# Optimization experiments

Measured on AMD Instinct MI355X. Metric: run time of the kernel, lower is better.

## Reference

```python
import jax, jax.numpy as jnp
import numpy as np

HIDDEN = 1024
B, S = 4, 2048

def setup_inputs() -> dict:
    key = jax.random.key(0)
    ks = jax.random.split(key, 8)
    scale = 1.0 / np.sqrt(HIDDEN)
    return {
        "x": jax.random.normal(ks[0], (B, S, HIDDEN), dtype=jnp.float32),
        "mask": jax.random.randint(ks[1], (B, S, S), 0, 2, dtype=jnp.int32),
        "Wq": jax.random.normal(ks[2], (HIDDEN, HIDDEN), dtype=jnp.float32) * scale,
        "bq": jax.random.normal(ks[3], (HIDDEN,), dtype=jnp.float32) * 0.01,
        "Wk": jax.random.normal(ks[4], (HIDDEN, HIDDEN), dtype=jnp.float32) * scale,
        "bk": jax.random.normal(ks[5], (HIDDEN,), dtype=jnp.float32) * 0.01,
        "Wv": jax.random.normal(ks[6], (HIDDEN, HIDDEN), dtype=jnp.float32) * scale,
        "bv": jax.random.normal(ks[7], (HIDDEN,), dtype=jnp.float32) * 0.01,
    }

def reference(x, mask, Wq, bq, Wk, bk, Wv, bv):
    # torch Linear: y = x @ W.T + b
    Q = jnp.einsum("bsh,oh->bso", x, Wq) + bq
    K = jnp.einsum("bsh,oh->bso", x, Wk) + bk
    V = jnp.einsum("bsh,oh->bso", x, Wv) + bv
    inv_sqrt_h = 1.0 / jnp.sqrt(jnp.asarray(Q.shape[-1], Q.dtype))
    score = jnp.einsum("bqh,bkh->bqk", Q, K) * inv_sqrt_h  # [B, S, S]
    score = jnp.where(mask == 0, jnp.asarray(-jnp.inf, score.dtype), score)
    attn = jax.nn.softmax(score, axis=-1)
    return jnp.einsum("bqk,bkh->bqh", attn, V)
```

## Files before the change

kernel.cpp:

```cpp
#include <hip/hip_runtime.h>

using u16 = unsigned short;
using u32 = unsigned int;

typedef __attribute__((ext_vector_type(4))) float f32x4;
typedef __attribute__((ext_vector_type(8))) short s16x8;

__device__ __forceinline__ u16 f2b(float f) {
  u32 u = __builtin_bit_cast(u32, f);
  u += 0x7FFFu + ((u >> 16) & 1u);
  return (u16)(u >> 16);
}
__device__ __forceinline__ float b2f(u16 h) {
  return __builtin_bit_cast(float, (u32)h << 16);
}
__device__ __forceinline__ void gl_lds16(const void* g, void* l) {
  __builtin_amdgcn_global_load_lds(
      (const __attribute__((address_space(1))) void*)g,
      (__attribute__((address_space(3))) void*)l, 16, 0, 0);
}
template<int N> __device__ __forceinline__ void waitvm() {
  static_assert(N == 8 || N == 6 || N == 4 || N == 3 || N == 0, "literal");
  if constexpr (N == 8)      asm volatile("s_waitcnt vmcnt(8)" ::: "memory");
  else if constexpr (N == 6) asm volatile("s_waitcnt vmcnt(6)" ::: "memory");
  else if constexpr (N == 4) asm volatile("s_waitcnt vmcnt(4)" ::: "memory");
  else if constexpr (N == 3) asm volatile("s_waitcnt vmcnt(3)" ::: "memory");
  else                       asm volatile("s_waitcnt vmcnt(0)" ::: "memory");
}
__device__ __forceinline__ void barrier_np() {
  __builtin_amdgcn_s_barrier();
  asm volatile("" ::: "memory");
}

__global__ __launch_bounds__(256) void convert4_k(
    const float* __restrict__ x, const float* __restrict__ Wq,
    const float* __restrict__ Wk, const float* __restrict__ Wv,
    u16* __restrict__ dst) {
  long g = (long)(blockIdx.x * 256 + threadIdx.x) * 8;
  const float* s;
  if (g < 8388608L)       s = x  + g;
  else if (g < 9437184L)  s = Wq + (g - 8388608L);
  else if (g < 10485760L) s = Wk + (g - 9437184L);
  else                    s = Wv + (g - 10485760L);
  f32x4 lo = *(const f32x4*)s;
  f32x4 hi = *(const f32x4*)(s + 4);
  s16x8 o;
  #pragma unroll
  for (int e = 0; e < 4; ++e) { o[e] = (short)f2b(lo[e]); o[4 + e] = (short)f2b(hi[e]); }
  *(s16x8*)(dst + g) = o;
}

template<int EPI, int MREP>
__global__ __launch_bounds__(512, 2) void gemm_nt(
    const u16* __restrict__ A, const u16* __restrict__ B0,
    const u16* __restrict__ W2, const u16* __restrict__ W3,
    int lda, int ldb, int K, long za, long zb, long ze,
    const float* __restrict__ bq, const float* __restrict__ bk, const float* __restrict__ bv,
    u16* __restrict__ qw, u16* __restrict__ kw, u16* __restrict__ vt,
    const int* __restrict__ mask, u16* __restrict__ sc, float* __restrict__ outO)
{
  constexpr int BM    = 32 * MREP;
  constexpr int ACH   = BM * 4;
  constexpr int CH    = ACH + 1024;
  constexpr int CALLS = CH / 512;
  constexpr int BUF   = CH * 8;
  __shared__ __align__(16) u16 lds[4 * BUF];

  const int tid  = threadIdx.x;
  const int wave = tid >> 6, lane = tid & 63;
  const int wr = wave >> 2, wc = wave & 3;
  const int m0 = blockIdx.y * BM, n0 = blockIdx.x * 256;
  const long z = blockIdx.z;
  A += z * za;

  const u16* Bsrc = B0;
  int nbase = n0;
  if constexpr (EPI == 0) {
    Bsrc = (n0 < 1024) ? B0 : (n0 < 2048) ? W2 : W3;
    nbase = n0 & 1023;
  }
  Bsrc += z * zb;

  const u16* gsrc[CALLS];
  u32 loff[CALLS];
  #pragma unroll
  for (int call = 0; call < CALLS; ++call) {
    int qq  = call * 512 + tid;
    int isB = qq >= ACH;
    int r   = (isB ? qq - ACH : qq) >> 2;
    int kc  = (qq & 3) ^ (r & 3);
    gsrc[call] = isB ? (Bsrc + (size_t)(nbase + r) * ldb + kc * 8)
                     : (A    + (size_t)(m0    + r) * lda + kc * 8);
    loff[call] = (u32)qq * 8;
  }

  const int frow = lane & 15;
  const int q    = lane >> 4;
  u32 aoff[MREP], boff[4];
  #pragma unroll
  for (int i = 0; i < MREP; ++i) {
    int lr = wr * (16 * MREP) + i * 16 + frow;
    aoff[i] = (u32)lr * 32 + (u32)((q ^ (lr & 3)) << 3);
  }
  #pragma unroll
  for (int j = 0; j < 4; ++j) {
    int lc = wc * 64 + j * 16 + frow;
    boff[j] = (u32)ACH * 8 + (u32)lc * 32 + (u32)((q ^ (lc & 3)) << 3);
  }

  f32x4 acc[MREP][4];
  const f32x4 fz = {0.f, 0.f, 0.f, 0.f};
  #pragma unroll
  for (int i = 0; i < MREP; ++i)
    #pragma unroll
    for (int j = 0; j < 4; ++j) acc[i][j] = fz;

  const int NT = K >> 5;

  auto stage = [&](int t) {
    u16* buf = lds + (size_t)(t & 3) * BUF;
    #pragma unroll
    for (int call = 0; call < CALLS; ++call)
      gl_lds16(gsrc[call] + (size_t)t * 32, buf + loff[call]);
  };
  auto comp = [&](int t) {
    const u16* buf = lds + (size_t)(t & 3) * BUF;
    s16x8 bf[4];
    #pragma unroll
    for (int j = 0; j < 4; ++j) bf[j] = *(const s16x8*)(buf + boff[j]);
    __builtin_amdgcn_s_setprio(1);
    #pragma unroll
    for (int i = 0; i < MREP; ++i) {
      s16x8 af = *(const s16x8*)(buf + aoff[i]);
      #pragma unroll
      for (int j = 0; j < 4; ++j)
        acc[i][j] = __builtin_amdgcn_mfma_f32_16x16x32_bf16(af, bf[j], acc[i][j], 0, 0, 0);
    }
    __builtin_amdgcn_s_setprio(0);
  };

  stage(0); stage(1); stage(2);
  for (int T = 0; T < NT - 3; ++T) {
    waitvm<2 * CALLS>();
    barrier_np();
    stage(T + 3);
    comp(T);
  }
  waitvm<2 * CALLS>(); barrier_np(); comp(NT - 3);
  waitvm<CALLS>();     barrier_np(); comp(NT - 2);
  waitvm<0>();         barrier_np(); comp(NT - 1);

  const int r0 = (lane >> 4) * 4;
  const int ccol = lane & 15;
  #pragma unroll
  for (int i = 0; i < MREP; ++i) {
    #pragma unroll
    for (int j = 0; j < 4; ++j) {
      #pragma unroll
      for (int r = 0; r < 4; ++r) {
        int R = m0 + wr * (16 * MREP) + i * 16 + r0 + r;
        int C = n0 + wc * 64 + j * 16 + ccol;
        float v = acc[i][j][r];
        if constexpr (EPI == 0) {
          int sec = C >> 10, nl = C & 1023;
          v += (sec == 0) ? bq[nl] : (sec == 1) ? bk[nl] : bv[nl];
          u16 o = f2b(v);
          int b = R >> 11, s = R & 2047;
          if (sec == 0)      qw[(size_t)R * 1024 + nl] = o;
          else if (sec == 1) kw[(size_t)R * 1024 + nl] = o;
          else               vt[(size_t)b * 2097152u + (size_t)nl * 2048 + s] = o;
        } else if constexpr (EPI == 1) {
          v *= 0.03125f;
          size_t idx = (size_t)(z * ze) + (size_t)R * 2048 + C;
          if (mask[idx] == 0) v = -__builtin_inff();
          sc[idx] = f2b(v);
        } else {
          outO[(size_t)(z * ze) + (size_t)R * 1024 + C] = v;
        }
      }
    }
  }
}

__global__ __launch_bounds__(256) void softmax_k(u16* __restrict__ Sc) {
  __shared__ float red[8];
  u16* p = Sc + (size_t)blockIdx.x * 2048;
  const int tid = threadIdx.x;
  const int lane = tid & 63, wv = tid >> 6;
  s16x8 u = *(const s16x8*)(p + tid * 8);
  float v[8];
  #pragma unroll
  for (int e = 0; e < 8; ++e) v[e] = b2f((u16)u[e]);
  float mx = v[0];
  #pragma unroll
  for (int e = 1; e < 8; ++e) mx = fmaxf(mx, v[e]);
  #pragma unroll
  for (int off = 32; off > 0; off >>= 1) mx = fmaxf(mx, __shfl_xor(mx, off));
  if (lane == 0) red[wv] = mx;
  __syncthreads();
  mx = fmaxf(fmaxf(red[0], red[1]), fmaxf(red[2], red[3]));
  float s = 0.f;
  #pragma unroll
  for (int e = 0; e < 8; ++e) { v[e] = __expf(v[e] - mx); s += v[e]; }
  #pragma unroll
  for (int off = 32; off > 0; off >>= 1) s += __shfl_xor(s, off);
  if (lane == 0) red[4 + wv] = s;
  __syncthreads();
  s = (red[4] + red[5]) + (red[6] + red[7]);
  float inv = 1.f / s;
  s16x8 o;
  #pragma unroll
  for (int e = 0; e < 8; ++e) o[e] = (short)f2b(v[e] * inv);
  *(s16x8*)(p + tid * 8) = o;
}

extern "C" void kernel_launch(void* const* d_in, const int* in_sizes, int n_in,
                              void* d_out, int out_size, void* d_ws, size_t ws_size,
                              hipStream_t stream) {
  const float* x  = (const float*)d_in[0];
  const int* mask = (const int*)d_in[1];
  const float* Wq = (const float*)d_in[2];
  const float* bq = (const float*)d_in[3];
  const float* Wk = (const float*)d_in[4];
  const float* bk = (const float*)d_in[5];
  const float* Wv = (const float*)d_in[6];
  const float* bv = (const float*)d_in[7];
  float* out = (float*)d_out;
  char* ws = (char*)d_ws;

  u16* xc  = (u16*)ws;
  u16* Wqc = (u16*)(ws + (16u << 20));
  u16* Wkc = (u16*)(ws + (18u << 20));
  u16* Wvc = (u16*)(ws + (20u << 20));
  u16* Qw  = (u16*)(ws + (22u << 20));
  u16* Kw  = (u16*)(ws + (38u << 20));
  u16* Vt  = (u16*)(ws + (54u << 20));
  u16* Sc  = (u16*)(ws + (70u << 20));

  convert4_k<<<5632, 256, 0, stream>>>(x, Wq, Wk, Wv, xc);

  gemm_nt<0, 4><<<dim3(12, 64, 1), 512, 0, stream>>>(
      xc, Wqc, Wkc, Wvc, 1024, 1024, 1024, 0, 0, 0,
      bq, bk, bv, Qw, Kw, Vt, nullptr, nullptr, nullptr);
  gemm_nt<1, 8><<<dim3(8, 8, 4), 512, 0, stream>>>(
      Qw, Kw, nullptr, nullptr, 1024, 1024, 1024, 2097152, 2097152, 4194304,
      nullptr, nullptr, nullptr, nullptr, nullptr, nullptr, mask, Sc, nullptr);
  softmax_k<<<8192, 256, 0, stream>>>(Sc);
  gemm_nt<2, 4><<<dim3(4, 16, 4), 512, 0, stream>>>(
      Sc, Vt, nullptr, nullptr, 2048, 2048, 2048, 4194304, 2097152, 2097152,
      nullptr, nullptr, nullptr, nullptr, nullptr, nullptr, nullptr, nullptr, out);
}
```

Before: 338.6 us.

## Split GEMM tile compute into two halves interleaved with staged loads and barriers

Restructures the GEMM main loop so each k-tile is processed in two halves. The global-to-LDS prefetch is split between them and issued after the LDS fragment reads, with an extra barrier per half, to spread memory issue across the MFMA work. It also changes the LDS swizzle to XOR on (row>>1)&3 to cut bank conflicts, and switches the QKV projection to MREP=8 (256-row tiles, half the blocks). The added barriers and larger tiles trade extra synchronisation and fewer blocks for better overlap and more reuse.

```diff
diff --git a/kernel.cpp b/kernel.cpp
--- a/kernel.cpp
+++ b/kernel.cpp
@@ -63,8 +63,10 @@
   constexpr int ACH   = BM * 4;
   constexpr int CH    = ACH + 1024;
   constexpr int CALLS = CH / 512;
-  constexpr int BUF   = CH * 8;
-  __shared__ __align__(16) u16 lds[4 * BUF];
+  constexpr int SA    = 2;
+  constexpr int SLOT  = CH * 8;
+  constexpr int HM    = MREP / 2;
+  __shared__ __align__(16) u16 lds[4 * SLOT];
 
   const int tid  = threadIdx.x;
   const int wave = tid >> 6, lane = tid & 63;
@@ -84,14 +86,14 @@
   const u16* gsrc[CALLS];
   u32 loff[CALLS];
   #pragma unroll
-  for (int call = 0; call < CALLS; ++call) {
-    int qq  = call * 512 + tid;
+  for (int c = 0; c < CALLS; ++c) {
+    int qq  = c * 512 + tid;
     int isB = qq >= ACH;
     int r   = (isB ? qq - ACH : qq) >> 2;
-    int kc  = (qq & 3) ^ (r & 3);
-    gsrc[call] = isB ? (Bsrc + (size_t)(nbase + r) * ldb + kc * 8)
-                     : (A    + (size_t)(m0    + r) * lda + kc * 8);
-    loff[call] = (u32)qq * 8;
+    int kc  = (qq & 3) ^ ((r >> 1) & 3);
+    gsrc[c] = (isB ? (Bsrc + (size_t)(nbase + r) * ldb)
+                   : (A    + (size_t)(m0    + r) * lda)) + kc * 8;
+    loff[c] = (u32)qq * 8;
   }
 
   const int frow = lane & 15;
@@ -100,12 +102,12 @@
   #pragma unroll
   for (int i = 0; i < MREP; ++i) {
     int lr = wr * (16 * MREP) + i * 16 + frow;
-    aoff[i] = (u32)lr * 32 + (u32)((q ^ (lr & 3)) << 3);
+    aoff[i] = (u32)lr * 32 + (u32)((q ^ ((lr >> 1) & 3)) << 3);
   }
   #pragma unroll
   for (int j = 0; j < 4; ++j) {
     int lc = wc * 64 + j * 16 + frow;
-    boff[j] = (u32)ACH * 8 + (u32)lc * 32 + (u32)((q ^ (lc & 3)) << 3);
+    boff[j] = (u32)ACH * 8 + (u32)lc * 32 + (u32)((q ^ ((lc >> 1) & 3)) << 3);
   }
 
   f32x4 acc[MREP][4];
@@ -117,38 +119,61 @@
 
   const int NT = K >> 5;
 
-  auto stage = [&](int t) {
-    u16* buf = lds + (size_t)(t & 3) * BUF;
-    #pragma unroll
-    for (int call = 0; call < CALLS; ++call)
-      gl_lds16(gsrc[call] + (size_t)t * 32, buf + loff[call]);
+  auto stage_full = [&](int t) {
+    u16* b = lds + (size_t)(t & 3) * SLOT;
+    #pragma unroll
+    for (int c = 0; c < CALLS; ++c)
+      gl_lds16(gsrc[c] + (size_t)t * 32, b + loff[c]);
   };
-  auto comp = [&](int t) {
-    const u16* buf = lds + (size_t)(t & 3) * BUF;
-    s16x8 bf[4];
+
+  s16x8 bf[4];
+  auto tile_body = [&](int T, bool do_stage) {
+    const u16* buf = lds + (size_t)(T & 3) * SLOT;
+    u16* sb = lds + (size_t)((T + 3) & 3) * SLOT;
+    const size_t koff = (size_t)(T + 3) * 32;
+    s16x8 af[HM];
     #pragma unroll
     for (int j = 0; j < 4; ++j) bf[j] = *(const s16x8*)(buf + boff[j]);
+    #pragma unroll
+    for (int i = 0; i < HM; ++i) af[i] = *(const s16x8*)(buf + aoff[i]);
+    if (do_stage) {
+      #pragma unroll
+      for (int c = 0; c < SA; ++c) gl_lds16(gsrc[c] + koff, sb + loff[c]);
+    }
+    barrier_np();
     __builtin_amdgcn_s_setprio(1);
     #pragma unroll
-    for (int i = 0; i < MREP; ++i) {
-      s16x8 af = *(const s16x8*)(buf + aoff[i]);
+    for (int i = 0; i < HM; ++i)
       #pragma unroll
       for (int j = 0; j < 4; ++j)
-        acc[i][j] = __builtin_amdgcn_mfma_f32_16x16x32_bf16(af, bf[j], acc[i][j], 0, 0, 0);
+        acc[i][j] = __builtin_amdgcn_mfma_f32_16x16x32_bf16(af[i], bf[j], acc[i][j], 0, 0, 0);
+    __builtin_amdgcn_s_setprio(0);
+    s16x8 ag[HM];
+    #pragma unroll
+    for (int i = 0; i < HM; ++i) ag[i] = *(const s16x8*)(buf + aoff[HM + i]);
+    if (do_stage) {
+      #pragma unroll
+      for (int c = SA; c < CALLS; ++c) gl_lds16(gsrc[c] + koff, sb + loff[c]);
     }
+    barrier_np();
+    __builtin_amdgcn_s_setprio(1);
+    #pragma unroll
+    for (int i = 0; i < HM; ++i)
+      #pragma unroll
+      for (int j = 0; j < 4; ++j)
+        acc[HM + i][j] = __builtin_amdgcn_mfma_f32_16x16x32_bf16(ag[i], bf[j], acc[HM + i][j], 0, 0, 0);
     __builtin_amdgcn_s_setprio(0);
   };
 
-  stage(0); stage(1); stage(2);
+  stage_full(0); stage_full(1); stage_full(2);
   for (int T = 0; T < NT - 3; ++T) {
     waitvm<2 * CALLS>();
     barrier_np();
-    stage(T + 3);
-    comp(T);
-  }
-  waitvm<2 * CALLS>(); barrier_np(); comp(NT - 3);
-  waitvm<CALLS>();     barrier_np(); comp(NT - 2);
-  waitvm<0>();         barrier_np(); comp(NT - 1);
+    tile_body(T, true);
+  }
+  waitvm<2 * CALLS>(); barrier_np(); tile_body(NT - 3, false);
+  waitvm<CALLS>();     barrier_np(); tile_body(NT - 2, false);
+  waitvm<0>();         barrier_np(); tile_body(NT - 1, false);
 
   const int r0 = (lane >> 4) * 4;
   const int ccol = lane & 15;
@@ -239,7 +264,7 @@
 
   convert4_k<<<5632, 256, 0, stream>>>(x, Wq, Wk, Wv, xc);
 
-  gemm_nt<0, 4><<<dim3(12, 64, 1), 512, 0, stream>>>(
+  gemm_nt<0, 8><<<dim3(12, 32, 1), 512, 0, stream>>>(
       xc, Wqc, Wkc, Wvc, 1024, 1024, 1024, 0, 0, 0,
       bq, bk, bv, Qw, Kw, Vt, nullptr, nullptr, nullptr);
   gemm_nt<1, 8><<<dim3(8, 8, 4), 512, 0, stream>>>(
```

Measured after the change: 330.7 us. 2.3% less time.

## Restructure GEMM main loop to 64-wide K tiles with phased double buffering

Applied to the files above, without the earlier changes.

The GEMM main loop now uses 64-wide K tiles with a two-buffer LDS ring instead of 32-wide tiles with a four-deep ring. The LDS swizzle is widened to 8 chunks to match. Each K tile is split into four phases. Each phase loads A fragments, issues one part of the next tile's A loads or the B loads two tiles ahead, then runs MFMAs between barriers, so global-to-LDS copies are spread across the compute. The aim is fewer wait/barrier rounds per unit of K and better overlap of loads with MFMAs. The cost is eight barriers per tile and tighter vmcnt bookkeeping, since B for tile t+2 is written into the buffer currently being read.

```diff
diff --git a/kernel.cpp b/kernel.cpp
--- a/kernel.cpp
+++ b/kernel.cpp
@@ -20,12 +20,9 @@
       (__attribute__((address_space(3))) void*)l, 16, 0, 0);
 }
 template<int N> __device__ __forceinline__ void waitvm() {
-  static_assert(N == 8 || N == 6 || N == 4 || N == 3 || N == 0, "literal");
-  if constexpr (N == 8)      asm volatile("s_waitcnt vmcnt(8)" ::: "memory");
-  else if constexpr (N == 6) asm volatile("s_waitcnt vmcnt(6)" ::: "memory");
-  else if constexpr (N == 4) asm volatile("s_waitcnt vmcnt(4)" ::: "memory");
-  else if constexpr (N == 3) asm volatile("s_waitcnt vmcnt(3)" ::: "memory");
-  else                       asm volatile("s_waitcnt vmcnt(0)" ::: "memory");
+  static_assert(N == 4 || N == 0, "literal");
+  if constexpr (N == 4) asm volatile("s_waitcnt vmcnt(4)" ::: "memory");
+  else                  asm volatile("s_waitcnt vmcnt(0)" ::: "memory");
 }
 __device__ __forceinline__ void barrier_np() {
   __builtin_amdgcn_s_barrier();
@@ -59,12 +56,14 @@
     u16* __restrict__ qw, u16* __restrict__ kw, u16* __restrict__ vt,
     const int* __restrict__ mask, u16* __restrict__ sc, float* __restrict__ outO)
 {
-  constexpr int BM    = 32 * MREP;
-  constexpr int ACH   = BM * 4;
-  constexpr int CH    = ACH + 1024;
-  constexpr int CALLS = CH / 512;
-  constexpr int BUF   = CH * 8;
-  __shared__ __align__(16) u16 lds[4 * BUF];
+  constexpr int BM   = 32 * MREP;
+  constexpr int WR   = 16 * MREP;
+  constexpr int RT   = MREP / 4;
+  constexpr int AU   = BM * 64;
+  constexpr int BU   = 256 * 64;
+  constexpr int BUFU = AU + BU;
+  constexpr int ACH  = BM / 128;
+  __shared__ __align__(16) u16 lds[2 * BUFU];
 
   const int tid  = threadIdx.x;
   const int wave = tid >> 6, lane = tid & 63;
@@ -81,31 +80,39 @@
   }
   Bsrc += z * zb;
 
-  const u16* gsrc[CALLS];
-  u32 loff[CALLS];
-  #pragma unroll
-  for (int call = 0; call < CALLS; ++call) {
-    int qq  = call * 512 + tid;
-    int isB = qq >= ACH;
-    int r   = (isB ? qq - ACH : qq) >> 2;
-    int kc  = (qq & 3) ^ (r & 3);
-    gsrc[call] = isB ? (Bsrc + (size_t)(nbase + r) * ldb + kc * 8)
-                     : (A    + (size_t)(m0    + r) * lda + kc * 8);
-    loff[call] = (u32)qq * 8;
+  const u16* pA[2 * ACH];
+  #pragma unroll
+  for (int hc = 0; hc < 2 * ACH; ++hc) {
+    int qq = hc * 512 + tid;
+    int r  = qq >> 3;
+    int cc = (qq & 7) ^ (r & 7);
+    pA[hc] = A + (size_t)(m0 + r) * lda + cc * 8;
+  }
+  const u16* pB[4];
+  #pragma unroll
+  for (int hc = 0; hc < 4; ++hc) {
+    int qq = hc * 512 + tid;
+    int r  = qq >> 3;
+    int cc = (qq & 7) ^ (r & 7);
+    pB[hc] = Bsrc + (size_t)(nbase + r) * ldb + cc * 8;
   }
 
   const int frow = lane & 15;
-  const int q    = lane >> 4;
-  u32 aoff[MREP], boff[4];
-  #pragma unroll
-  for (int i = 0; i < MREP; ++i) {
-    int lr = wr * (16 * MREP) + i * 16 + frow;
-    aoff[i] = (u32)lr * 32 + (u32)((q ^ (lr & 3)) << 3);
+  const int lq   = lane >> 4;
+  u32 aoff[MREP][2], boff[4][2];
+  #pragma unroll
+  for (int rt = 0; rt < MREP; ++rt) {
+    int lr = wr * WR + rt * 16 + frow;
+    #pragma unroll
+    for (int s = 0; s < 2; ++s)
+      aoff[rt][s] = (u32)lr * 64 + (u32)(((s * 4 + lq) ^ (lr & 7)) << 3);
   }
   #pragma unroll
   for (int j = 0; j < 4; ++j) {
     int lc = wc * 64 + j * 16 + frow;
-    boff[j] = (u32)ACH * 8 + (u32)lc * 32 + (u32)((q ^ (lc & 3)) << 3);
+    #pragma unroll
+    for (int s = 0; s < 2; ++s)
+      boff[j][s] = (u32)AU + (u32)lc * 64 + (u32)(((s * 4 + lq) ^ (lc & 7)) << 3);
   }
 
   f32x4 acc[MREP][4];
@@ -115,40 +122,69 @@
     #pragma unroll
     for (int j = 0; j < 4; ++j) acc[i][j] = fz;
 
-  const int NT = K >> 5;
-
-  auto stage = [&](int t) {
-    u16* buf = lds + (size_t)(t & 3) * BUF;
-    #pragma unroll
-    for (int call = 0; call < CALLS; ++call)
-      gl_lds16(gsrc[call] + (size_t)t * 32, buf + loff[call]);
+  const int NT = K >> 6;
+
+  auto stageA = [&](int t, int h) {
+    u16* d = lds + (size_t)(t & 1) * BUFU;
+    #pragma unroll
+    for (int c = 0; c < ACH; ++c) {
+      int hc = h * ACH + c;
+      gl_lds16(pA[hc] + (size_t)t * 64, d + hc * 4096 + tid * 8);
+    }
   };
-  auto comp = [&](int t) {
-    const u16* buf = lds + (size_t)(t & 3) * BUF;
-    s16x8 bf[4];
-    #pragma unroll
-    for (int j = 0; j < 4; ++j) bf[j] = *(const s16x8*)(buf + boff[j]);
-    __builtin_amdgcn_s_setprio(1);
-    #pragma unroll
-    for (int i = 0; i < MREP; ++i) {
-      s16x8 af = *(const s16x8*)(buf + aoff[i]);
+  auto stageB = [&](int t, int h) {
+    u16* d = lds + (size_t)(t & 1) * BUFU + AU;
+    #pragma unroll
+    for (int c = 0; c < 2; ++c) {
+      int hc = h * 2 + c;
+      gl_lds16(pB[hc] + (size_t)t * 64, d + hc * 4096 + tid * 8);
+    }
+  };
+
+  stageA(0, 0); stageA(0, 1);
+  stageB(0, 0); stageB(0, 1);
+  stageB(1, 0); stageB(1, 1);
+  waitvm<4>();
+  barrier_np();
+
+  for (int t = 0; t < NT; ++t) {
+    const u16* buf = lds + (size_t)(t & 1) * BUFU;
+    s16x8 bf[4][2];
+    #pragma unroll
+    for (int p = 0; p < 4; ++p) {
+      if (p == 0) {
+        #pragma unroll
+        for (int j = 0; j < 4; ++j)
+          #pragma unroll
+          for (int s = 0; s < 2; ++s) bf[j][s] = *(const s16x8*)(buf + boff[j][s]);
+      }
+      s16x8 af[RT][2];
       #pragma unroll
-      for (int j = 0; j < 4; ++j)
-        acc[i][j] = __builtin_amdgcn_mfma_f32_16x16x32_bf16(af, bf[j], acc[i][j], 0, 0, 0);
-    }
-    __builtin_amdgcn_s_setprio(0);
-  };
-
-  stage(0); stage(1); stage(2);
-  for (int T = 0; T < NT - 3; ++T) {
-    waitvm<2 * CALLS>();
-    barrier_np();
-    stage(T + 3);
-    comp(T);
-  }
-  waitvm<2 * CALLS>(); barrier_np(); comp(NT - 3);
-  waitvm<CALLS>();     barrier_np(); comp(NT - 2);
-  waitvm<0>();         barrier_np(); comp(NT - 1);
+      for (int i = 0; i < RT; ++i)
+        #pragma unroll
+        for (int s = 0; s < 2; ++s)
+          af[i][s] = *(const s16x8*)(buf + aoff[p * RT + i][s]);
+      if (p == 0) { if (t + 1 < NT) stageA(t + 1, 0); }
+      if (p == 1) { if (t + 1 < NT) stageA(t + 1, 1); }
+      if (p == 2) { if (t + 2 < NT) stageB(t + 2, 0); }
+      if (p == 3) {
+        if (t + 2 < NT) { stageB(t + 2, 1); waitvm<4>(); }
+        else if (t + 1 < NT) { waitvm<0>(); }
+      }
+      barrier_np();
+      __builtin_amdgcn_s_setprio(1);
+      #pragma unroll
+      for (int i = 0; i < RT; ++i)
+        #pragma unroll
+        for (int j = 0; j < 4; ++j)
+          #pragma unroll
+          for (int s = 0; s < 2; ++s)
+            acc[p * RT + i][j] =
+                __builtin_amdgcn_mfma_f32_16x16x32_bf16(af[i][s], bf[j][s], acc[p * RT + i][j], 0, 0, 0);
+      __builtin_amdgcn_s_setprio(0);
+      barrier_np();
+    }
+  }
 
   const int r0 = (lane >> 4) * 4;
   const int ccol = lane & 15;
@@ -158,7 +194,7 @@
     for (int j = 0; j < 4; ++j) {
       #pragma unroll
       for (int r = 0; r < 4; ++r) {
-        int R = m0 + wr * (16 * MREP) + i * 16 + r0 + r;
+        int R = m0 + wr * WR + i * 16 + r0 + r;
         int C = n0 + wc * 64 + j * 16 + ccol;
         float v = acc[i][j][r];
         if constexpr (EPI == 0) {
```

After: 334.5 us. About the same (-1.2%).
